# Optimization experiments

Measured on AMD Instinct MI355X. Metric: run time of the kernel, lower is better.

Reference implementation:

```python
import jax, jax.numpy as jnp
import numpy as np

N_HEAD = 16
D = 1024
LV = 2048
HEAD_DIM = D // N_HEAD
B = 2
LQ = 2048
LN_EPS = 1e-5


def setup_inputs() -> dict:
    key = jax.random.key(0)
    ks = jax.random.split(key, 8)
    s = 0.02
    v = jax.random.normal(ks[0], (B, LV, D), dtype=jnp.float32)
    q = jax.random.normal(ks[1], (B, LQ, D), dtype=jnp.float32)
    # per-head attn linear: d -> lv
    Wa = jax.random.normal(ks[2], (N_HEAD, D, LV), dtype=jnp.float32) * s
    ba = jnp.zeros((N_HEAD, LV), dtype=jnp.float32)
    # per-head layernorm over d
    gamma = jnp.ones((N_HEAD, D), dtype=jnp.float32)
    beta = jnp.zeros((N_HEAD, D), dtype=jnp.float32)
    # per-head proj (FilteredLinear modeled as affine): d -> head_dim
    Wp = jax.random.normal(ks[3], (N_HEAD, D, HEAD_DIM), dtype=jnp.float32) * s
    bp = jnp.zeros((N_HEAD, HEAD_DIM), dtype=jnp.float32)
    return {"v": v, "q": q, "Wa": Wa, "ba": ba, "gamma": gamma,
            "beta": beta, "Wp": Wp, "bp": bp}


def _mha(v, q, Wa, ba, gamma, beta, Wp, bp):
    # attn: [H, B, Lq, Lv] = relu(q @ Wa_h + ba_h)  (batched across heads)
    attn = jax.nn.relu(jnp.einsum('bqd,hdl->hbql', q, Wa)
                       + ba[:, None, None, :])
    # external-attention aggregation: [H, B, Lq, D]
    agg = jnp.einsum('hbql,bld->hbqd', attn, v)
    # per-head LayerNorm over last dim (d)
    mu = jnp.mean(agg, axis=-1, keepdims=True)
    var = jnp.var(agg, axis=-1, keepdims=True)
    normed = (agg - mu) * jax.lax.rsqrt(var + LN_EPS)
    normed = normed * gamma[:, None, None, :] + beta[:, None, None, :]
    # per-head projection to head_dim: [H, B, Lq, head_dim]
    heads = jnp.einsum('hbqd,hde->hbqe', normed, Wp) + bp[:, None, None, :]
    # concat heads along feature dim -> [B, Lq, D]
    return heads.transpose(1, 2, 0, 3).reshape(q.shape[0], q.shape[1], -1)


def reference(v, q, Wa, ba, gamma, beta, Wp, bp):
    return _mha(v, q, Wa, ba, gamma, beta, Wp, bp)
```

## Files before the change

kernel.cpp:

```cpp
#include <hip/hip_runtime.h>
#include <hip/hip_bf16.h>

typedef __attribute__((ext_vector_type(8))) short short8;
typedef __attribute__((ext_vector_type(4))) float f32x4;

#define N_HEAD 16
#define DMODEL 1024
#define LV 2048
#define LQ 2048
#define BATCH 2
#define HEAD_DIM 64

template <int N> struct IC { static constexpr int v = N; };

__device__ inline ushort f2bf(float f) {
    union { float f; unsigned u; } v; v.f = f;
    unsigned r = v.u + 0x7fffu + ((v.u >> 16) & 1u);
    return (ushort)(r >> 16);
}
__device__ inline float bf2f(ushort h) {
    union { unsigned u; float f; } v; v.u = ((unsigned)h) << 16;
    return v.f;
}

__global__ __launch_bounds__(256) void cast_bf16(const float* __restrict__ src,
                                                 ushort* __restrict__ dst, int n) {
    int i = (blockIdx.x * 256 + threadIdx.x) * 4;
    if (i < n) {
        float4 v = *(const float4*)(src + i);
        ushort4 o;
        o.x = f2bf(v.x); o.y = f2bf(v.y); o.z = f2bf(v.z); o.w = f2bf(v.w);
        *(ushort4*)(dst + i) = o;
    }
}

__global__ __launch_bounds__(256) void transpose_cast(const float* __restrict__ src,
                                                      ushort* __restrict__ dst,
                                                      int R, int C) {
    __shared__ float t[32][33];
    size_t zoff = (size_t)blockIdx.z * R * C;
    int c0 = blockIdx.x * 32, r0 = blockIdx.y * 32;
    int tx = threadIdx.x, ty = threadIdx.y;
#pragma unroll
    for (int i = 0; i < 4; ++i)
        t[ty + i * 8][tx] = src[zoff + (size_t)(r0 + ty + i * 8) * C + c0 + tx];
    __syncthreads();
#pragma unroll
    for (int i = 0; i < 4; ++i)
        dst[zoff + (size_t)(c0 + ty + i * 8) * R + r0 + tx] = f2bf(t[tx][ty + i * 8]);
}

template <bool RELU>
__global__ __launch_bounds__(512, 2) void gemm256(
    const ushort* __restrict__ A, const ushort* __restrict__ B,
    ushort* __restrict__ Cout, const float* __restrict__ bias,
    int K,
    long sA_b, long sA_h, long sB_b, long sB_h, long sC_z, int ldc, long sBias_h)
{
    __shared__ __align__(16) char smem[131072];

    const int z = blockIdx.z, b = z & 1, h = z >> 1;
    A += (size_t)b * sA_b + (size_t)h * sA_h;
    B += (size_t)b * sB_b + (size_t)h * sB_h;
    const float* biasp = bias ? bias + (size_t)h * sBias_h : nullptr;

    const int bm0 = blockIdx.y * 256;
    const int bn0 = blockIdx.x * 256;
    const int T = threadIdx.x;
    const int lane = T & 63, wid = T >> 6;
    const int wr = wid >> 2, wc = wid & 3;
    const int fr = lane & 15, fq = lane >> 4;
    const int laneoff = fr * 64 + ((fq * 16) ^ ((fr >> 3) << 5));

    const char* pA0 = smem + 0     + wr * 8192 + laneoff;
    const char* pB0 = smem + 32768 + wc * 4096 + laneoff;
    const char* pA1 = pA0 + 65536;
    const char* pB1 = pB0 + 65536;

    const int s_row = T >> 2;
    const int s_csw = ((T & 3) * 16) ^ (((T >> 5) & 1) << 5);
    const ushort* gA = A + (size_t)(bm0 + s_row) * K + (s_csw >> 1);
    const ushort* gB = B + (size_t)(bn0 + s_row) * K + (s_csw >> 1);

    const int nt = K >> 6;

    auto stage = [&](int op, int kh, int db, int snext) {
        const ushort* g = op ? gB : gA;
        const size_t kbase = (size_t)snext * 64 + kh * 32;
        char* d = smem + db * 65536 + op * 32768 + kh * 16384 + (T << 4);
#pragma unroll
        for (int j = 0; j < 2; ++j) {
            __builtin_amdgcn_global_load_lds(
                (const __attribute__((address_space(1))) void*)(g + (size_t)j * 128 * K + kbase),
                (__attribute__((address_space(3))) void*)(d + j * 8192), 16, 0, 0);
        }
    };

    f32x4 acc[8][4];
#pragma unroll
    for (int m = 0; m < 8; ++m)
#pragma unroll
        for (int n = 0; n < 4; ++n)
#pragma unroll
            for (int j = 0; j < 4; ++j) acc[m][n][j] = 0.f;

    auto phase = [&](const char* pA, const char* pB, short8* bfr, int s, int db,
                     auto MH, auto KH, auto RDB, auto DOST, auto SOP, auto SKH, auto VM) {
        constexpr int mh = decltype(MH)::v, kh = decltype(KH)::v;
        short8 a[4];
#pragma unroll
        for (int i = 0; i < 4; ++i)
            a[i] = *(const short8*)(pA + kh * 16384 + (mh * 4 + i) * 1024);
        if constexpr (decltype(RDB)::v) {
#pragma unroll
            for (int n = 0; n < 4; ++n)
                bfr[n] = *(const short8*)(pB + kh * 16384 + n * 1024);
        }
        if constexpr (decltype(DOST)::v)
            stage(decltype(SOP)::v, decltype(SKH)::v, db ^ 1, s + 1);
        asm volatile("s_barrier" ::: "memory");
        asm volatile("s_waitcnt lgkmcnt(0)" ::: "memory");
        __builtin_amdgcn_sched_barrier(0);
        __builtin_amdgcn_s_setprio(1);
#pragma unroll
        for (int i = 0; i < 4; ++i)
#pragma unroll
            for (int n = 0; n < 4; ++n)
                acc[mh * 4 + i][n] = __builtin_amdgcn_mfma_f32_16x16x32_bf16(
                    a[i], bfr[n], acc[mh * 4 + i][n], 0, 0, 0);
        __builtin_amdgcn_s_setprio(0);
        __builtin_amdgcn_sched_barrier(0);
        constexpr int vm = decltype(VM)::v;
        if constexpr (vm == 4) asm volatile("s_waitcnt vmcnt(4)" ::: "memory");
        else if constexpr (vm == 0) asm volatile("s_waitcnt vmcnt(0)" ::: "memory");
        asm volatile("s_barrier" ::: "memory");
    };

    auto step_full = [&](int s, const char* pA, const char* pB, int db) {
        short8 bfr[4];
        phase(pA, pB, bfr, s, db, IC<0>{}, IC<0>{}, IC<1>{}, IC<1>{}, IC<0>{}, IC<0>{}, IC<-1>{});
        phase(pA, pB, bfr, s, db, IC<1>{}, IC<0>{}, IC<0>{}, IC<1>{}, IC<1>{}, IC<0>{}, IC<4>{});
        phase(pA, pB, bfr, s, db, IC<0>{}, IC<1>{}, IC<1>{}, IC<1>{}, IC<0>{}, IC<1>{}, IC<-1>{});
        phase(pA, pB, bfr, s, db, IC<1>{}, IC<1>{}, IC<0>{}, IC<1>{}, IC<1>{}, IC<1>{}, IC<4>{});
    };
    auto step_last = [&](int s, const char* pA, const char* pB, int db) {
        short8 bfr[4];
        phase(pA, pB, bfr, s, db, IC<0>{}, IC<0>{}, IC<1>{}, IC<0>{}, IC<0>{}, IC<0>{}, IC<-1>{});
        phase(pA, pB, bfr, s, db, IC<1>{}, IC<0>{}, IC<0>{}, IC<0>{}, IC<0>{}, IC<0>{}, IC<0>{});
        phase(pA, pB, bfr, s, db, IC<0>{}, IC<1>{}, IC<1>{}, IC<0>{}, IC<0>{}, IC<0>{}, IC<-1>{});
        phase(pA, pB, bfr, s, db, IC<1>{}, IC<1>{}, IC<0>{}, IC<0>{}, IC<0>{}, IC<0>{}, IC<-1>{});
    };

    stage(0, 0, 0, 0); stage(1, 0, 0, 0); stage(0, 1, 0, 0); stage(1, 1, 0, 0);
    asm volatile("s_waitcnt vmcnt(4)" ::: "memory");
    asm volatile("s_barrier" ::: "memory");

    for (int s = 0; s < nt - 2; s += 2) {
        step_full(s,     pA0, pB0, 0);
        step_full(s + 1, pA1, pB1, 1);
    }
    step_full(nt - 2, pA0, pB0, 0);
    step_last(nt - 1, pA1, pB1, 1);

    ushort* C = Cout + (size_t)z * sC_z;
    const int row0 = bm0 + wr * 128;
    const int col0 = bn0 + wc * 64;
#pragma unroll
    for (int n = 0; n < 4; ++n) {
        const int c = col0 + n * 16 + fr;
        const float bvv = biasp ? biasp[c] : 0.f;
#pragma unroll
        for (int m = 0; m < 8; ++m) {
            const int r = row0 + m * 16 + fq * 4;
#pragma unroll
            for (int j = 0; j < 4; ++j) {
                float val = acc[m][n][j] + bvv;
                if (RELU) val = fmaxf(val, 0.f);
                C[(size_t)(r + j) * ldc + c] = f2bf(val);
            }
        }
    }
}

__global__ __launch_bounds__(256) void ln_kernel(ushort* __restrict__ agg,
                                                 const float* __restrict__ gamma,
                                                 const float* __restrict__ beta) {
    const int wid = threadIdx.x >> 6, lane = threadIdx.x & 63;
    const size_t row = (size_t)blockIdx.x * 4 + wid;
    const int h = (int)(row >> 12);
    ushort* p = agg + row * 1024 + lane * 16;
    short8 r0 = *(const short8*)p;
    short8 r1 = *(const short8*)(p + 8);
    float x[16];
#pragma unroll
    for (int j = 0; j < 8; ++j) { x[j] = bf2f((ushort)r0[j]); x[8 + j] = bf2f((ushort)r1[j]); }
    float s = 0.f, s2 = 0.f;
#pragma unroll
    for (int j = 0; j < 16; ++j) { s += x[j]; s2 += x[j] * x[j]; }
    for (int o = 1; o < 64; o <<= 1) {
        s  += __shfl_xor(s,  o, 64);
        s2 += __shfl_xor(s2, o, 64);
    }
    float mu  = s * (1.0f / 1024.0f);
    float var = s2 * (1.0f / 1024.0f) - mu * mu;
    float rs  = rsqrtf(fmaxf(var, 0.f) + 1e-5f);
    const float* g  = gamma + (size_t)h * 1024 + lane * 16;
    const float* bt = beta  + (size_t)h * 1024 + lane * 16;
    short8 o0, o1;
#pragma unroll
    for (int j = 0; j < 8; ++j) {
        o0[j] = (short)f2bf((x[j]     - mu) * rs * g[j]     + bt[j]);
        o1[j] = (short)f2bf((x[8 + j] - mu) * rs * g[8 + j] + bt[8 + j]);
    }
    *(short8*)p = o0;
    *(short8*)(p + 8) = o1;
}

__global__ __launch_bounds__(256) void proj_kernel(const ushort* __restrict__ normed,
                                                   const ushort* __restrict__ WpT,
                                                   const float* __restrict__ bp,
                                                   float* __restrict__ out,
                                                   int h_base) {
    const int z = blockIdx.y, b = z & 1, h = z >> 1;
    const int hg = h_base + h;
    const int wid = threadIdx.x >> 6, lane = threadIdx.x & 63;
    const int fr = lane & 15, fq = lane >> 4;
    const int m0 = (blockIdx.x * 4 + wid) * 16;

    const ushort* Abase = normed + ((size_t)z * 2048 + m0 + fr) * 1024 + fq * 8;
    const ushort* Bbase = WpT + (size_t)hg * 64 * 1024 + (size_t)fr * 1024 + fq * 8;

    f32x4 acc[4];
#pragma unroll
    for (int n = 0; n < 4; ++n)
#pragma unroll
        for (int j = 0; j < 4; ++j) acc[n][j] = 0.f;

    for (int kt = 0; kt < 32; ++kt) {
        short8 a = *(const short8*)(Abase + kt * 32);
#pragma unroll
        for (int n = 0; n < 4; ++n) {
            short8 bb = *(const short8*)(Bbase + n * 16 * 1024 + kt * 32);
            acc[n] = __builtin_amdgcn_mfma_f32_16x16x32_bf16(a, bb, acc[n], 0, 0, 0);
        }
    }
#pragma unroll
    for (int n = 0; n < 4; ++n) {
        int c = hg * 64 + n * 16 + fr;
        float bvv = bp[hg * 64 + n * 16 + fr];
#pragma unroll
        for (int j = 0; j < 4; ++j)
            out[(size_t)b * 2048 * 1024 + (size_t)(m0 + fq * 4 + j) * 1024 + c] =
                acc[n][j] + bvv;
    }
}

extern "C" void kernel_launch(void* const* d_in, const int* in_sizes, int n_in,
                              void* d_out, int out_size, void* d_ws, size_t ws_size,
                              hipStream_t stream) {
    const float* v     = (const float*)d_in[0];
    const float* q     = (const float*)d_in[1];
    const float* Wa    = (const float*)d_in[2];
    const float* ba    = (const float*)d_in[3];
    const float* gamma = (const float*)d_in[4];
    const float* beta  = (const float*)d_in[5];
    const float* Wp    = (const float*)d_in[6];
    const float* bp    = (const float*)d_in[7];
    float* out = (float*)d_out;

    const size_t MB = 1ull << 20;
    char* ws = (char*)d_ws;
    ushort* qbf = (ushort*)(ws);
    ushort* vT  = (ushort*)(ws + 8 * MB);
    ushort* WpT = (ushort*)(ws + 16 * MB);
    int NH = 1;
    {
        const int cands[5] = {16, 8, 4, 2, 1};
        for (int i = 0; i < 5; ++i) {
            if ((size_t)(18 + 28 * cands[i]) * MB <= ws_size) { NH = cands[i]; break; }
        }
    }
    ushort* WaT_c  = (ushort*)(ws + 18 * MB);
    ushort* attn_c = (ushort*)(ws + (18 + (size_t)4 * NH) * MB);
    ushort* agg_c  = (ushort*)(ws + (18 + (size_t)20 * NH) * MB);

    dim3 tb(32, 8);
    cast_bf16<<<4096, 256, 0, stream>>>(q, qbf, BATCH * LQ * DMODEL);
    transpose_cast<<<dim3(DMODEL / 32, LV / 32, BATCH), tb, 0, stream>>>(v, vT, LV, DMODEL);
    transpose_cast<<<dim3(HEAD_DIM / 32, DMODEL / 32, N_HEAD), tb, 0, stream>>>(Wp, WpT, DMODEL, HEAD_DIM);

    for (int h0 = 0; h0 < N_HEAD; h0 += NH) {
        transpose_cast<<<dim3(LV / 32, DMODEL / 32, NH), tb, 0, stream>>>(
            Wa + (size_t)h0 * DMODEL * LV, WaT_c, DMODEL, LV);

        gemm256<true><<<dim3(LV / 256, LQ / 256, NH * 2), 512, 0, stream>>>(
            qbf, WaT_c, attn_c, ba + (size_t)h0 * LV, DMODEL,
            (long)LQ * DMODEL, 0L,
            0L, (long)LV * DMODEL,
            (long)LQ * LV, LV, (long)LV);

        gemm256<false><<<dim3(DMODEL / 256, LQ / 256, NH * 2), 512, 0, stream>>>(
            attn_c, vT, agg_c, nullptr, LV,
            (long)LQ * LV, (long)2 * LQ * LV,
            (long)DMODEL * LV, 0L,
            (long)LQ * DMODEL, DMODEL, 0L);

        ln_kernel<<<(NH * 2 * LQ) / 4, 256, 0, stream>>>(
            agg_c, gamma + (size_t)h0 * DMODEL, beta + (size_t)h0 * DMODEL);

        proj_kernel<<<dim3(LQ / 64, NH * 2), 256, 0, stream>>>(
            agg_c, WpT, bp, out, h0);
    }
}
```

Baseline: 817.0 us.

## Shrink GEMM tile to 128x256 with triple-buffered K=32 LDS pipeline

Replaces the 256x256 double-buffered GEMM (K step 64, 128KB LDS) with a 128x256 tile that uses a three-stage ring of 24KB LDS buffers at K step 32, prefetching two steps ahead. Halving the accumulators and LDS footprint targets more resident blocks per CU (launch bounds raised to 4 waves-per-EU hint) and a deeper prefetch to hide global latency. In exchange, each block gets less operand reuse per tile (more global/L2 traffic for the B operand), and the barrier-per-step with a smaller K slice adds more synchronization overhead relative to MFMA work.

```diff
diff --git a/kernel.cpp b/kernel.cpp
--- a/kernel.cpp
+++ b/kernel.cpp
@@ -51,20 +51,20 @@
 }
 
 template <bool RELU>
-__global__ __launch_bounds__(512, 2) void gemm256(
+__global__ __launch_bounds__(512, 4) void gemm128x256(
     const ushort* __restrict__ A, const ushort* __restrict__ B,
     ushort* __restrict__ Cout, const float* __restrict__ bias,
     int K,
     long sA_b, long sA_h, long sB_b, long sB_h, long sC_z, int ldc, long sBias_h)
 {
-    __shared__ __align__(16) char smem[131072];
+    __shared__ __align__(16) char smem[3 * 24576];
 
     const int z = blockIdx.z, b = z & 1, h = z >> 1;
     A += (size_t)b * sA_b + (size_t)h * sA_h;
     B += (size_t)b * sB_b + (size_t)h * sB_h;
     const float* biasp = bias ? bias + (size_t)h * sBias_h : nullptr;
 
-    const int bm0 = blockIdx.y * 256;
+    const int bm0 = blockIdx.y * 128;
     const int bn0 = blockIdx.x * 256;
     const int T = threadIdx.x;
     const int lane = T & 63, wid = T >> 6;
@@ -72,105 +72,87 @@
     const int fr = lane & 15, fq = lane >> 4;
     const int laneoff = fr * 64 + ((fq * 16) ^ ((fr >> 3) << 5));
 
-    const char* pA0 = smem + 0     + wr * 8192 + laneoff;
-    const char* pB0 = smem + 32768 + wc * 4096 + laneoff;
-    const char* pA1 = pA0 + 65536;
-    const char* pB1 = pB0 + 65536;
-
     const int s_row = T >> 2;
     const int s_csw = ((T & 3) * 16) ^ (((T >> 5) & 1) << 5);
     const ushort* gA = A + (size_t)(bm0 + s_row) * K + (s_csw >> 1);
     const ushort* gB = B + (size_t)(bn0 + s_row) * K + (s_csw >> 1);
 
-    const int nt = K >> 6;
-
-    auto stage = [&](int op, int kh, int db, int snext) {
-        const ushort* g = op ? gB : gA;
-        const size_t kbase = (size_t)snext * 64 + kh * 32;
-        char* d = smem + db * 65536 + op * 32768 + kh * 16384 + (T << 4);
+    const int nt = K >> 5;
+
+    auto stage = [&](int sb, int kt) {
+        char* base = smem + sb * 24576;
+        const ushort* srcA = gA + (size_t)kt * 32;
+        __builtin_amdgcn_global_load_lds(
+            (const __attribute__((address_space(1))) void*)srcA,
+            (__attribute__((address_space(3))) void*)(base + (T << 4)), 16, 0, 0);
 #pragma unroll
         for (int j = 0; j < 2; ++j) {
+            const ushort* srcB = gB + (size_t)j * 128 * K + (size_t)kt * 32;
             __builtin_amdgcn_global_load_lds(
-                (const __attribute__((address_space(1))) void*)(g + (size_t)j * 128 * K + kbase),
-                (__attribute__((address_space(3))) void*)(d + j * 8192), 16, 0, 0);
+                (const __attribute__((address_space(1))) void*)srcB,
+                (__attribute__((address_space(3))) void*)(base + 8192 + j * 8192 + (T << 4)),
+                16, 0, 0);
         }
     };
 
-    f32x4 acc[8][4];
-#pragma unroll
-    for (int m = 0; m < 8; ++m)
+    f32x4 acc[4][4];
+#pragma unroll
+    for (int m = 0; m < 4; ++m)
 #pragma unroll
         for (int n = 0; n < 4; ++n)
 #pragma unroll
             for (int j = 0; j < 4; ++j) acc[m][n][j] = 0.f;
 
-    auto phase = [&](const char* pA, const char* pB, short8* bfr, int s, int db,
-                     auto MH, auto KH, auto RDB, auto DOST, auto SOP, auto SKH, auto VM) {
-        constexpr int mh = decltype(MH)::v, kh = decltype(KH)::v;
-        short8 a[4];
-#pragma unroll
-        for (int i = 0; i < 4; ++i)
-            a[i] = *(const short8*)(pA + kh * 16384 + (mh * 4 + i) * 1024);
-        if constexpr (decltype(RDB)::v) {
-#pragma unroll
-            for (int n = 0; n < 4; ++n)
-                bfr[n] = *(const short8*)(pB + kh * 16384 + n * 1024);
-        }
-        if constexpr (decltype(DOST)::v)
-            stage(decltype(SOP)::v, decltype(SKH)::v, db ^ 1, s + 1);
-        asm volatile("s_barrier" ::: "memory");
+    auto step = [&](int t, int rb, int sb, auto DOST, auto VM) {
+        const char* base = smem + rb * 24576;
+        const char* pA = base + wr * 4096 + laneoff;
+        const char* pB = base + 8192 + wc * 4096 + laneoff;
+        short8 a[4], bb[4];
+#pragma unroll
+        for (int m = 0; m < 4; ++m) a[m] = *(const short8*)(pA + m * 1024);
+#pragma unroll
+        for (int n = 0; n < 4; ++n) bb[n] = *(const short8*)(pB + n * 1024);
+        if constexpr (decltype(DOST)::v) stage(sb, t + 2);
         asm volatile("s_waitcnt lgkmcnt(0)" ::: "memory");
         __builtin_amdgcn_sched_barrier(0);
         __builtin_amdgcn_s_setprio(1);
 #pragma unroll
-        for (int i = 0; i < 4; ++i)
+        for (int m = 0; m < 4; ++m)
 #pragma unroll
             for (int n = 0; n < 4; ++n)
-                acc[mh * 4 + i][n] = __builtin_amdgcn_mfma_f32_16x16x32_bf16(
-                    a[i], bfr[n], acc[mh * 4 + i][n], 0, 0, 0);
+                acc[m][n] = __builtin_amdgcn_mfma_f32_16x16x32_bf16(
+                    a[m], bb[n], acc[m][n], 0, 0, 0);
         __builtin_amdgcn_s_setprio(0);
         __builtin_amdgcn_sched_barrier(0);
         constexpr int vm = decltype(VM)::v;
-        if constexpr (vm == 4) asm volatile("s_waitcnt vmcnt(4)" ::: "memory");
+        if constexpr (vm == 3) asm volatile("s_waitcnt vmcnt(3)" ::: "memory");
         else if constexpr (vm == 0) asm volatile("s_waitcnt vmcnt(0)" ::: "memory");
-        asm volatile("s_barrier" ::: "memory");
+        if constexpr (vm >= 0) asm volatile("s_barrier" ::: "memory");
     };
 
-    auto step_full = [&](int s, const char* pA, const char* pB, int db) {
-        short8 bfr[4];
-        phase(pA, pB, bfr, s, db, IC<0>{}, IC<0>{}, IC<1>{}, IC<1>{}, IC<0>{}, IC<0>{}, IC<-1>{});
-        phase(pA, pB, bfr, s, db, IC<1>{}, IC<0>{}, IC<0>{}, IC<1>{}, IC<1>{}, IC<0>{}, IC<4>{});
-        phase(pA, pB, bfr, s, db, IC<0>{}, IC<1>{}, IC<1>{}, IC<1>{}, IC<0>{}, IC<1>{}, IC<-1>{});
-        phase(pA, pB, bfr, s, db, IC<1>{}, IC<1>{}, IC<0>{}, IC<1>{}, IC<1>{}, IC<1>{}, IC<4>{});
-    };
-    auto step_last = [&](int s, const char* pA, const char* pB, int db) {
-        short8 bfr[4];
-        phase(pA, pB, bfr, s, db, IC<0>{}, IC<0>{}, IC<1>{}, IC<0>{}, IC<0>{}, IC<0>{}, IC<-1>{});
-        phase(pA, pB, bfr, s, db, IC<1>{}, IC<0>{}, IC<0>{}, IC<0>{}, IC<0>{}, IC<0>{}, IC<0>{});
-        phase(pA, pB, bfr, s, db, IC<0>{}, IC<1>{}, IC<1>{}, IC<0>{}, IC<0>{}, IC<0>{}, IC<-1>{});
-        phase(pA, pB, bfr, s, db, IC<1>{}, IC<1>{}, IC<0>{}, IC<0>{}, IC<0>{}, IC<0>{}, IC<-1>{});
-    };
-
-    stage(0, 0, 0, 0); stage(1, 0, 0, 0); stage(0, 1, 0, 0); stage(1, 1, 0, 0);
-    asm volatile("s_waitcnt vmcnt(4)" ::: "memory");
+    stage(0, 0); stage(1, 1);
+    asm volatile("s_waitcnt vmcnt(3)" ::: "memory");
     asm volatile("s_barrier" ::: "memory");
 
-    for (int s = 0; s < nt - 2; s += 2) {
-        step_full(s,     pA0, pB0, 0);
-        step_full(s + 1, pA1, pB1, 1);
-    }
-    step_full(nt - 2, pA0, pB0, 0);
-    step_last(nt - 1, pA1, pB1, 1);
+    int rb = 0, sb = 2;
+    for (int t = 0; t < nt - 2; ++t) {
+        step(t, rb, sb, IC<1>{}, IC<3>{});
+        rb = (rb == 2) ? 0 : rb + 1;
+        sb = (sb == 2) ? 0 : sb + 1;
+    }
+    step(nt - 2, rb, sb, IC<0>{}, IC<0>{});
+    rb = (rb == 2) ? 0 : rb + 1;
+    step(nt - 1, rb, sb, IC<0>{}, IC<-1>{});
 
     ushort* C = Cout + (size_t)z * sC_z;
-    const int row0 = bm0 + wr * 128;
+    const int row0 = bm0 + wr * 64;
     const int col0 = bn0 + wc * 64;
 #pragma unroll
     for (int n = 0; n < 4; ++n) {
         const int c = col0 + n * 16 + fr;
         const float bvv = biasp ? biasp[c] : 0.f;
 #pragma unroll
-        for (int m = 0; m < 8; ++m) {
+        for (int m = 0; m < 4; ++m) {
             const int r = row0 + m * 16 + fq * 4;
 #pragma unroll
             for (int j = 0; j < 4; ++j) {
@@ -293,13 +275,13 @@
         transpose_cast<<<dim3(LV / 32, DMODEL / 32, NH), tb, 0, stream>>>(
             Wa + (size_t)h0 * DMODEL * LV, WaT_c, DMODEL, LV);
 
-        gemm256<true><<<dim3(LV / 256, LQ / 256, NH * 2), 512, 0, stream>>>(
+        gemm128x256<true><<<dim3(LV / 256, LQ / 128, NH * 2), 512, 0, stream>>>(
             qbf, WaT_c, attn_c, ba + (size_t)h0 * LV, DMODEL,
             (long)LQ * DMODEL, 0L,
             0L, (long)LV * DMODEL,
             (long)LQ * LV, LV, (long)LV);
 
-        gemm256<false><<<dim3(DMODEL / 256, LQ / 256, NH * 2), 512, 0, stream>>>(
+        gemm128x256<false><<<dim3(DMODEL / 256, LQ / 128, NH * 2), 512, 0, stream>>>(
             attn_c, vT, agg_c, nullptr, LV,
             (long)LQ * LV, (long)2 * LQ * LV,
             (long)DMODEL * LV, 0L,
```

After: 845.3 us. +3.5%, slower.
